# Optimization experiments

Hardware: AMD Instinct MI355X
Metric: run time of the kernel (lower is better)

The kernel has to match this reference:

```python
import jax, jax.numpy as jnp
import numpy as np

B, T, D_MODEL = 2, 2048, 1024
H, D = 16, 64
NEG = -1e9


def setup_inputs() -> dict:
    key = jax.random.key(0)
    k1, k2, k3 = jax.random.split(key, 3)
    x = jax.random.normal(k1, (B, T, D_MODEL), dtype=jnp.float32)
    # causal additive bias: 0 at valid (j<=i), large negative otherwise
    causal = jnp.tril(jnp.ones((T, T), dtype=bool))
    mask = jnp.where(causal, 0.0, NEG).astype(jnp.float32)[None, None]
    # params (torch Linear no-bias; stored as [in, out] so y = x @ W)
    W_qkv = jax.random.normal(k2, (D_MODEL, H * 5 * D), dtype=jnp.float32) / np.sqrt(D_MODEL)
    W_out = jax.random.normal(k3, (H * D, D_MODEL), dtype=jnp.float32) / np.sqrt(H * D)
    lam = jnp.full((H,), 0.8, dtype=jnp.float32)
    return {"x": x, "mask": mask, "W_qkv": W_qkv, "W_out": W_out, "lam": lam}


def reference(x, mask, W_qkv, W_out, lam):
    scale = np.sqrt(D).astype(np.float32)
    qkv = (x @ W_qkv).reshape(B, T, H, 5 * D)          # (B,T,H,5D)
    q1, q2, k1, k2, v = (qkv[..., i * D:(i + 1) * D] for i in range(5))
    # scores: (B,H,T,T)
    s1 = jnp.einsum('bihd,bjhd->bhij', q1, k1) / scale + mask
    s2 = jnp.einsum('bihd,bjhd->bhij', q2, k2) / scale + mask
    a1 = jax.nn.softmax(s1, axis=-1)
    a2 = jax.nn.softmax(s2, axis=-1)
    lam_c = jnp.clip(lam, 0.0, 1.0)[None, :, None, None]
    attn = a1 - lam_c * a2
    out = jnp.einsum('bhij,bjhd->bihd', attn, v).reshape(B, T, H * D)
    return out @ W_out
```

## Files before the change

kernel.cpp:

```cpp
#include <hip/hip_runtime.h>


typedef __attribute__((ext_vector_type(8))) short short8;
typedef __attribute__((ext_vector_type(4))) short short4v;
typedef __attribute__((ext_vector_type(4))) float floatx4;
typedef __attribute__((ext_vector_type(2))) unsigned uintx2;

#define MFMA16(A_, B_, C_) __builtin_amdgcn_mfma_f32_16x16x32_bf16((A_), (B_), (C_), 0, 0, 0)

#if __has_builtin(__builtin_amdgcn_mfma_f32_16x16x16_bf16)
#define PVMFMA(A_, B_, C_) __builtin_amdgcn_mfma_f32_16x16x16_bf16((A_), (B_), (C_), 0, 0, 0)
#elif __has_builtin(__builtin_amdgcn_mfma_f32_16x16x16bf16_1k)
#define PVMFMA(A_, B_, C_) __builtin_amdgcn_mfma_f32_16x16x16bf16_1k((A_), (B_), (C_), 0, 0, 0)
#else
__device__ __forceinline__ floatx4 pvmfma_asm(short4v a, short4v b, floatx4 c) {
  asm("v_mfma_f32_16x16x16_bf16 %0, %1, %2, %0\n\ts_nop 7" : "+v"(c) : "v"(a), "v"(b));
  return c;
}
#define PVMFMA(A_, B_, C_) pvmfma_asm((A_), (B_), (C_))
#endif

__device__ __forceinline__ unsigned short f2bf(float f) {
  unsigned u;
  __builtin_memcpy(&u, &f, 4);
  u += 0x7fffu + ((u >> 16) & 1u);
  return (unsigned short)(u >> 16);
}

__device__ __forceinline__ unsigned packbf2(float a, float b) {
  unsigned ua, ub;
  __builtin_memcpy(&ua, &a, 4);
  __builtin_memcpy(&ub, &b, 4);
  ua += 0x8000u;
  ub += 0x8000u;
  return __builtin_amdgcn_perm(ub, ua, 0x07060302u);
}

__device__ __forceinline__ void gload16(const unsigned short* g, void* l) {
  __builtin_amdgcn_global_load_lds(
      (const __attribute__((address_space(1))) void*)g,
      (__attribute__((address_space(3))) void*)l, 16, 0, 0);
}

__global__ __launch_bounds__(256) void prep(const float* __restrict__ x,
                                            unsigned short* __restrict__ xb,
                                            const float* __restrict__ wqkv,
                                            unsigned short* __restrict__ wqkvT,
                                            const float* __restrict__ wout,
                                            unsigned short* __restrict__ woutT) {
  int bid = blockIdx.x;
  if (bid < 2048) {
    size_t i = ((size_t)bid * 256 + threadIdx.x) * 8;
    float4 a0 = *(const float4*)(x + i);
    float4 a1 = *(const float4*)(x + i + 4);
    short8 v = {(short)f2bf(a0.x), (short)f2bf(a0.y), (short)f2bf(a0.z), (short)f2bf(a0.w),
                (short)f2bf(a1.x), (short)f2bf(a1.y), (short)f2bf(a1.z), (short)f2bf(a1.w)};
    *(short8*)(xb + i) = v;
    return;
  }
  bid -= 2048;
  __shared__ unsigned short t[32][33];
  const float* in;
  unsigned short* out;
  int R = 1024, C;
  int bx, by;
  if (bid < 5120) {
    in = wqkv; out = wqkvT; C = 5120;
    bx = bid % 160; by = bid / 160;
  } else {
    bid -= 5120;
    in = wout; out = woutT; C = 1024;
    bx = bid % 32; by = bid / 32;
  }
  int c0 = bx * 32, r0 = by * 32;
  int tx = threadIdx.x & 31, ty = threadIdx.x >> 5;
#pragma unroll
  for (int i = 0; i < 4; i++) {
    int r = ty + i * 8;
    t[r][tx] = f2bf(in[(size_t)(r0 + r) * C + c0 + tx]);
  }
  __syncthreads();
#pragma unroll
  for (int i = 0; i < 4; i++) {
    int r = ty + i * 8;
    out[(size_t)(c0 + r) * R + r0 + tx] = t[tx][r];
  }
}

__global__ __launch_bounds__(512, 2) void gemm_qkv(const unsigned short* __restrict__ A,
                                                   const unsigned short* __restrict__ Bt,
                                                   unsigned short* __restrict__ qkbuf,
                                                   unsigned short* __restrict__ vtbuf) {
  const int tid = threadIdx.x;
  const int wave = tid >> 6, lane = tid & 63, lane15 = lane & 15, quad = lane >> 4;
  const int wm = wave >> 2, wn = wave & 3;
  const int bn = blockIdx.x & 15, bm = blockIdx.x >> 4;
  const int row0 = bm * 256, col0 = bn * 320;
  __shared__ __align__(16) short SMEM[73728];
  floatx4 acc[8][5] = {};

  const int srow = lane >> 3;
  const int sseg = ((lane & 7) ^ srow) * 8;
  const unsigned short* gA = A + (size_t)(row0 + srow) * 1024 + sseg;
  const unsigned short* gB = Bt + (size_t)(col0 + srow) * 1024 + sseg;

  auto stage = [&](int buf, int t) {
#pragma unroll
    for (int u = 0; u < 4; u++) {
      const int c = wave * 4 + u;
      gload16(gA + (size_t)c * 8192 + t * 64, &SMEM[buf * 16384 + c * 512]);
    }
#pragma unroll
    for (int u = 0; u < 5; u++) {
      const int c = wave * 5 + u;
      gload16(gB + (size_t)c * 8192 + t * 64, &SMEM[32768 + buf * 20480 + c * 512]);
    }
  };

  stage(0, 0);
  stage(1, 1);

  const int swz = (lane15 & 7) << 3;
  for (int t = 0; t < 16; t++) {
    if (t < 15) {
      asm volatile("s_waitcnt vmcnt(9)" ::: "memory");
    } else {
      asm volatile("s_waitcnt vmcnt(0)" ::: "memory");
    }
    __builtin_amdgcn_s_barrier();
    const short* Ab = &SMEM[(t & 1) * 16384];
    const short* Bb = &SMEM[32768 + (t & 1) * 20480];
#pragma unroll
    for (int kh = 0; kh < 2; kh++) {
      short8 bf[5];
#pragma unroll
      for (int nt = 0; nt < 5; nt++)
        bf[nt] =
            *(const short8*)&Bb[(wn * 80 + nt * 16 + lane15) * 64 + ((kh * 32 + quad * 8) ^ swz)];
#pragma unroll
      for (int mh = 0; mh < 2; mh++) {
        short8 af[4];
#pragma unroll
        for (int mt = 0; mt < 4; mt++)
          af[mt] = *(const short8*)&Ab[(wm * 128 + mh * 64 + mt * 16 + lane15) * 64 +
                                       ((kh * 32 + quad * 8) ^ swz)];
        __builtin_amdgcn_s_setprio(1);
#pragma unroll
        for (int mt = 0; mt < 4; mt++)
#pragma unroll
          for (int nt = 0; nt < 5; nt++)
            acc[mh * 4 + mt][nt] = MFMA16(af[mt], bf[nt], acc[mh * 4 + mt][nt]);
        __builtin_amdgcn_s_setprio(0);
      }
    }
    __builtin_amdgcn_s_barrier();
    if (t + 2 < 16) stage(t & 1, t + 2);
  }

  const int h = bn;
  short* Svt = SMEM;
#pragma unroll
  for (int m = 0; m < 8; m++) {
    const int row = row0 + wm * 128 + m * 16 + quad * 4;
#pragma unroll
    for (int nt = 0; nt < 5; nt++) {
      const int local = wn * 80 + nt * 16 + lane15;
      if (local < 256) {
        const float qs = (local < 128) ? 0.18033688011112042f : 1.0f;
#pragma unroll
        for (int r = 0; r < 4; r++)
          qkbuf[(size_t)(row + r) * 4096 + h * 256 + local] = f2bf(acc[m][nt][r] * qs);
      } else {
        const int d = local - 256;
#pragma unroll
        for (int r = 0; r < 4; r++)
          Svt[d * 264 + wm * 128 + m * 16 + quad * 4 + r] = (short)f2bf(acc[m][nt][r]);
      }
    }
  }
  __syncthreads();
  {
    const int bb = row0 >> 11, t0 = row0 & 2047;
    const int d = tid >> 3, sg = (tid & 7) * 32;
    unsigned short* gdst = vtbuf + (size_t)((bb * 16 + h) * 64 + d) * 2048 + t0 + sg;
#pragma unroll
    for (int u2 = 0; u2 < 4; u2++)
      *(short8*)(gdst + u2 * 8) = *(const short8*)&Svt[d * 264 + sg + u2 * 8];
  }
}

__global__ __launch_bounds__(512, 4) void attn_kernel(const unsigned short* __restrict__ qk,
                                                      const unsigned short* __restrict__ vt,
                                                      const float* __restrict__ lam,
                                                      unsigned short* __restrict__ attnout) {
  const int tid = threadIdx.x;
  const int wave = tid >> 6, lane = tid & 63, lane15 = lane & 15, quad = lane >> 4;
  const int w4 = wave & 3, wt = wave >> 2;
  const int bid = blockIdx.x;
  const int u = bid >> 8, c = bid & 255, k = c >> 5, bh = c & 31;
  const int pr = u ? (15 - k) : k;
  const int h = bh & 15, b = bh >> 4;
  const int qt = wt ? (31 - pr) : pr;

  __shared__ __align__(16) short K12s[2][64 * 128];
  __shared__ __align__(16) short Vts[2][64 * 64];
  __shared__ __align__(16) short Ls[8][16 * 68];

  const float lamv = fminf(fmaxf(lam[h], 0.0f), 1.0f);

  const unsigned short* kbase = qk + (size_t)(b * 2048) * 4096 + h * 256 + 128;
  const unsigned short* vbase = vt + (size_t)((b * 16 + h) * 64) * 2048;

  const int klr = lane >> 4, kcp = (lane & 15) * 16;
  const int vlr = lane >> 3, vcp = (lane & 7) * 16;
  const int swz = (lane15 & 7) << 4;

  auto stageKV = [&](int buf, int jt) {
#pragma unroll
    for (int u2 = 0; u2 < 2; u2++) {
      const int ck = wave * 2 + u2, row = 4 * ck + klr;
      gload16(kbase + (size_t)(jt * 64 + row) * 4096 + ((kcp ^ ((row & 7) << 4)) >> 1),
              &K12s[buf][ck * 512]);
    }
    {
      const int cv = wave, row = 8 * cv + vlr;
      gload16(vbase + (size_t)row * 2048 + jt * 64 + ((vcp ^ ((row & 7) << 4)) >> 1),
              &Vts[buf][cv * 512]);
    }
  };

  const int qrow0 = qt * 64 + w4 * 16;
  const unsigned short* qb = qk + (size_t)(b * 2048 + qrow0 + lane15) * 4096 + h * 256;
  const short8 q1f0 = *(const short8*)(qb + quad * 8);
  const short8 q1f1 = *(const short8*)(qb + 32 + quad * 8);
  const short8 q2f0 = *(const short8*)(qb + 64 + quad * 8);
  const short8 q2f1 = *(const short8*)(qb + 96 + quad * 8);

  floatx4 o1[4] = {}, o2[4] = {};
  float lp1 = 0.f, lp2 = 0.f;

  const int qsub = qt * 4 + w4;
  const int njt = 32 - pr;

  stageKV(0, 0);
  stageKV(1, 1);

  for (int jt = 0; jt < njt; jt++) {
    if (jt + 1 < njt) {
      asm volatile("s_waitcnt vmcnt(3)" ::: "memory");
    } else {
      asm volatile("s_waitcnt vmcnt(0)" ::: "memory");
    }
    __builtin_amdgcn_s_barrier();

    const int cur = jt & 1;
    const int rel = qsub - 4 * jt;
    if (rel >= 0) {
#pragma unroll
      for (int mat = 0; mat < 2; mat++) {
        const int koffB = mat ? 128 : 0;
        const short8 qf0 = mat ? q2f0 : q1f0;
        const short8 qf1 = mat ? q2f1 : q1f1;
        float* lp = mat ? &lp2 : &lp1;
        floatx4* oo = mat ? o2 : o1;

#pragma unroll
        for (int ms = 0; ms < 4; ms++) {
          if (ms <= rel) {
            const short* kr = &K12s[cur][(ms * 16 + lane15) * 128];
            short8 k0 = *(const short8*)(kr + (((koffB + quad * 16) ^ swz) >> 1));
            short8 k1 = *(const short8*)(kr + (((koffB + 64 + quad * 16) ^ swz) >> 1));
            floatx4 s = {0.f, 0.f, 0.f, 0.f};
            s = MFMA16(k0, qf0, s);
            s = MFMA16(k1, qf1, s);
            float e[4];
#pragma unroll
            for (int r = 0; r < 4; r++) e[r] = __builtin_amdgcn_exp2f(s[r]);
            if (ms == rel) {
              const int jq = quad * 4;
#pragma unroll
              for (int r = 0; r < 4; r++) e[r] = (jq + r <= lane15) ? e[r] : 0.0f;
            }
            *lp += (e[0] + e[1]) + (e[2] + e[3]);
            uintx2 wv = {packbf2(e[0], e[1]), packbf2(e[2], e[3])};
            short4v bv;
            __builtin_memcpy(&bv, &wv, 8);
            const int vcol = ((ms * 32 + quad * 8) ^ swz) >> 1;
#pragma unroll
            for (int nt = 0; nt < 4; nt++) {
              const short4v av = *(const short4v*)&Vts[cur][(nt * 16 + lane15) * 64 + vcol];
              oo[nt] = PVMFMA(av, bv, oo[nt]);
            }
          }
        }
      }
    }
    asm volatile("s_waitcnt lgkmcnt(0)" ::: "memory");
    __builtin_amdgcn_s_barrier();
    if (jt + 2 < njt) stageKV(cur, jt + 2);
  }

  lp1 += __shfl_xor(lp1, 16, 64);
  lp1 += __shfl_xor(lp1, 32, 64);
  lp2 += __shfl_xor(lp2, 16, 64);
  lp2 += __shfl_xor(lp2, 32, 64);

  const float rl1 = __builtin_amdgcn_rcpf(lp1);
  const float rl2 = lamv * __builtin_amdgcn_rcpf(lp2);
  short* L = &Ls[wave][0];
#pragma unroll
  for (int nt = 0; nt < 4; nt++) {
    float v0 = o1[nt][0] * rl1 - o2[nt][0] * rl2;
    float v1 = o1[nt][1] * rl1 - o2[nt][1] * rl2;
    float v2 = o1[nt][2] * rl1 - o2[nt][2] * rl2;
    float v3 = o1[nt][3] * rl1 - o2[nt][3] * rl2;
    uintx2 wv = {packbf2(v0, v1), packbf2(v2, v3)};
    *(uintx2*)&L[lane15 * 68 + nt * 16 + quad * 4] = wv;
  }
#pragma unroll
  for (int r2 = 0; r2 < 4; r2++) {
    const uintx2 ov = *(const uintx2*)&L[(quad * 4 + r2) * 68 + lane15 * 4];
    const int row = b * 2048 + qrow0 + quad * 4 + r2;
    *(uintx2*)&attnout[(size_t)row * 1024 + h * 64 + lane15 * 4] = ov;
  }
}

__global__ __launch_bounds__(256) void gemm_out(const unsigned short* __restrict__ A,
                                                const unsigned short* __restrict__ Bt,
                                                float* __restrict__ Cout) {
  const int tid = threadIdx.x;
  const int wave = tid >> 6, lane = tid & 63, lane15 = lane & 15, quad = lane >> 4;
  const int wr = wave >> 1, wc = wave & 1;
  const int bn = blockIdx.x & 7, bm = blockIdx.x >> 3;
  const int row0 = bm * 64, col0 = bn * 128;
  __shared__ __align__(16) short As[64 * 64];
  __shared__ __align__(16) short Bs[128 * 64];
  floatx4 acc[2][4] = {};
  const int slr = lane >> 3, scl = (lane & 7) * 8;
  for (int kt = 0; kt < 1024; kt += 64) {
    __syncthreads();
#pragma unroll
    for (int u = 0; u < 2; u++) {
      const int c = wave * 2 + u;
      gload16(A + (size_t)(row0 + 8 * c + slr) * 1024 + kt + scl, &As[c * 512]);
    }
#pragma unroll
    for (int u = 0; u < 4; u++) {
      const int c = wave * 4 + u;
      gload16(Bt + (size_t)(col0 + 8 * c + slr) * 1024 + kt + scl, &Bs[c * 512]);
    }
    __syncthreads();
#pragma unroll
    for (int kh = 0; kh < 2; kh++) {
      short8 af[2], bf[4];
#pragma unroll
      for (int mt = 0; mt < 2; mt++)
        af[mt] = *(const short8*)&As[(wr * 32 + mt * 16 + lane15) * 64 + kh * 32 + quad * 8];
#pragma unroll
      for (int nt = 0; nt < 4; nt++)
        bf[nt] = *(const short8*)&Bs[(wc * 64 + nt * 16 + lane15) * 64 + kh * 32 + quad * 8];
#pragma unroll
      for (int mt = 0; mt < 2; mt++)
#pragma unroll
        for (int nt = 0; nt < 4; nt++) acc[mt][nt] = MFMA16(af[mt], bf[nt], acc[mt][nt]);
    }
  }
#pragma unroll
  for (int mt = 0; mt < 2; mt++)
#pragma unroll
    for (int nt = 0; nt < 4; nt++)
#pragma unroll
      for (int r = 0; r < 4; r++) {
        int row = row0 + wr * 32 + mt * 16 + quad * 4 + r;
        int col = col0 + wc * 64 + nt * 16 + lane15;
        Cout[(size_t)row * 1024 + col] = acc[mt][nt][r];
      }
}

extern "C" void kernel_launch(void* const* d_in, const int* in_sizes, int n_in,
                              void* d_out, int out_size, void* d_ws, size_t ws_size,
                              hipStream_t stream) {
  const float* x = (const float*)d_in[0];
  const float* Wqkv = (const float*)d_in[2];
  const float* Wout = (const float*)d_in[3];
  const float* lam = (const float*)d_in[4];
  float* out = (float*)d_out;

  unsigned short* ws = (unsigned short*)d_ws;
  unsigned short* WqkvT = ws;
  unsigned short* WoutT = WqkvT + (size_t)5120 * 1024;
  unsigned short* qkbuf = WoutT + (size_t)1024 * 1024;
  unsigned short* vtbuf = qkbuf + (size_t)4096 * 4096;
  unsigned short* xb = vtbuf + (size_t)2 * 16 * 64 * 2048;
  unsigned short* attnbuf = xb;

  prep<<<2048 + 6144, 256, 0, stream>>>(x, xb, Wqkv, WqkvT, Wout, WoutT);
  gemm_qkv<<<16 * 16, 512, 0, stream>>>(xb, WqkvT, qkbuf, vtbuf);
  attn_kernel<<<512, 512, 0, stream>>>(qkbuf, vtbuf, lam, attnbuf);
  gemm_out<<<64 * 8, 256, 0, stream>>>(attnbuf, WoutT, out);
}
```

Before: 226.2 us.

## Double-buffer output GEMM with swizzled LDS and async prefetch

Rewrites the output projection GEMM so it stages two k-tiles ahead into double-buffered shared memory, using explicit vmcnt waits and barriers in place of full syncthreads. The global-to-LDS loads use an XOR swizzle so the MFMA operand reads avoid bank conflicts, and it adds setprio around the MFMA block plus a two-blocks-per-CU launch bound. The aim is to overlap global loads with compute in the final GEMM. In exchange it uses 48KB of LDS per block and relies on manual waitcnt accounting being correct.

```diff
diff --git a/kernel.cpp b/kernel.cpp
--- a/kernel.cpp
+++ b/kernel.cpp
@@ -325,46 +325,70 @@
   }
 }
 
-__global__ __launch_bounds__(256) void gemm_out(const unsigned short* __restrict__ A,
-                                                const unsigned short* __restrict__ Bt,
-                                                float* __restrict__ Cout) {
+__global__ __launch_bounds__(256, 2) void gemm_out(const unsigned short* __restrict__ A,
+                                                   const unsigned short* __restrict__ Bt,
+                                                   float* __restrict__ Cout) {
   const int tid = threadIdx.x;
   const int wave = tid >> 6, lane = tid & 63, lane15 = lane & 15, quad = lane >> 4;
   const int wr = wave >> 1, wc = wave & 1;
   const int bn = blockIdx.x & 7, bm = blockIdx.x >> 3;
   const int row0 = bm * 64, col0 = bn * 128;
-  __shared__ __align__(16) short As[64 * 64];
-  __shared__ __align__(16) short Bs[128 * 64];
+  __shared__ __align__(16) short SMEM[24576];
   floatx4 acc[2][4] = {};
-  const int slr = lane >> 3, scl = (lane & 7) * 8;
-  for (int kt = 0; kt < 1024; kt += 64) {
-    __syncthreads();
+
+  const int srow = lane >> 3;
+  const int sseg = ((lane & 7) ^ srow) * 8;
+  const unsigned short* gA = A + (size_t)(row0 + srow) * 1024 + sseg;
+  const unsigned short* gB = Bt + (size_t)(col0 + srow) * 1024 + sseg;
+
+  auto stage = [&](int buf, int t) {
 #pragma unroll
     for (int u = 0; u < 2; u++) {
       const int c = wave * 2 + u;
-      gload16(A + (size_t)(row0 + 8 * c + slr) * 1024 + kt + scl, &As[c * 512]);
+      gload16(gA + (size_t)c * 8192 + t * 64, &SMEM[buf * 4096 + c * 512]);
     }
 #pragma unroll
     for (int u = 0; u < 4; u++) {
       const int c = wave * 4 + u;
-      gload16(Bt + (size_t)(col0 + 8 * c + slr) * 1024 + kt + scl, &Bs[c * 512]);
-    }
-    __syncthreads();
+      gload16(gB + (size_t)c * 8192 + t * 64, &SMEM[8192 + buf * 8192 + c * 512]);
+    }
+  };
+
+  stage(0, 0);
+  stage(1, 1);
+
+  const int swz = (lane15 & 7) << 3;
+  for (int t = 0; t < 16; t++) {
+    if (t < 15) {
+      asm volatile("s_waitcnt vmcnt(6)" ::: "memory");
+    } else {
+      asm volatile("s_waitcnt vmcnt(0)" ::: "memory");
+    }
+    __builtin_amdgcn_s_barrier();
+    const short* Ab = &SMEM[(t & 1) * 4096];
+    const short* Bb = &SMEM[8192 + (t & 1) * 8192];
 #pragma unroll
     for (int kh = 0; kh < 2; kh++) {
       short8 af[2], bf[4];
 #pragma unroll
       for (int mt = 0; mt < 2; mt++)
-        af[mt] = *(const short8*)&As[(wr * 32 + mt * 16 + lane15) * 64 + kh * 32 + quad * 8];
+        af[mt] =
+            *(const short8*)&Ab[(wr * 32 + mt * 16 + lane15) * 64 + ((kh * 32 + quad * 8) ^ swz)];
 #pragma unroll
       for (int nt = 0; nt < 4; nt++)
-        bf[nt] = *(const short8*)&Bs[(wc * 64 + nt * 16 + lane15) * 64 + kh * 32 + quad * 8];
+        bf[nt] =
+            *(const short8*)&Bb[(wc * 64 + nt * 16 + lane15) * 64 + ((kh * 32 + quad * 8) ^ swz)];
+      __builtin_amdgcn_s_setprio(1);
 #pragma unroll
       for (int mt = 0; mt < 2; mt++)
 #pragma unroll
         for (int nt = 0; nt < 4; nt++) acc[mt][nt] = MFMA16(af[mt], bf[nt], acc[mt][nt]);
-    }
-  }
+      __builtin_amdgcn_s_setprio(0);
+    }
+    __builtin_amdgcn_s_barrier();
+    if (t + 2 < 16) stage(t & 1, t + 2);
+  }
+
 #pragma unroll
   for (int mt = 0; mt < 2; mt++)
 #pragma unroll
```

Result: faster. 215.8 us (-4.6%).
